# Performance work log

Measured on AMD Instinct MI355X. Metric: run time of the kernel, lower is better.

## Reference

```python
import jax, jax.numpy as jnp
import numpy as np

N_NODES = 50000
N_EDGES = 800000
HIDDEN = 128


def setup_inputs() -> dict:
    key = jax.random.key(0)
    k_emb, k_ei, k1, k2, k3, kb1, kb2, kb3 = jax.random.split(key, 8)
    emb = jax.random.normal(k_emb, (N_NODES, HIDDEN), dtype=jnp.float32)
    edge_index = jax.random.randint(k_ei, (2, N_EDGES), 0, N_NODES, dtype=jnp.int64)
    h = HIDDEN
    # MLP([2h, 4h, h, 1]) weights, Kaiming-uniform-ish init
    def lin(k, fan_in, fan_out):
        bound = 1.0 / np.sqrt(fan_in)
        return jax.random.uniform(k, (fan_in, fan_out), jnp.float32, -bound, bound)
    W1 = lin(k1, 2 * h, 4 * h)
    b1 = jax.random.uniform(kb1, (4 * h,), jnp.float32, -1.0 / np.sqrt(2 * h), 1.0 / np.sqrt(2 * h))
    W2 = lin(k2, 4 * h, h)
    b2 = jax.random.uniform(kb2, (h,), jnp.float32, -1.0 / np.sqrt(4 * h), 1.0 / np.sqrt(4 * h))
    W3 = lin(k3, h, 1)
    b3 = jax.random.uniform(kb3, (1,), jnp.float32, -1.0 / np.sqrt(h), 1.0 / np.sqrt(h))
    return {"emb": emb, "edge_index": edge_index,
            "W1": W1, "b1": b1, "W2": W2, "b2": b2, "W3": W3, "b3": b3}


def reference(emb, edge_index, W1, b1, W2, b2, W3, b3):
    # learn_edge_att=True path: gather endpoints, concat, 3-layer MLP
    col, row = edge_index[0], edge_index[1]
    f12 = jnp.concatenate([emb[col], emb[row]], axis=-1)  # [E, 2h]
    x = jax.nn.relu(f12 @ W1 + b1)                         # [E, 4h]
    x = jax.nn.relu(x @ W2 + b2)                           # [E, h]
    att_log_logits = x @ W3 + b3                           # [E, 1]
    return att_log_logits
```

## Files before the change

### kernel.cpp

```cpp
#include <hip/hip_runtime.h>
#include <hip/hip_bf16.h>
#include <stdint.h>

#define N_EDGES   800000
#define N_NODESC  50000
#define HID       128

typedef __attribute__((ext_vector_type(8))) short bf16x8;
typedef __attribute__((ext_vector_type(4))) float f32x4;
typedef __attribute__((ext_vector_type(4))) unsigned int u32x4;

__device__ __forceinline__ short f2bf(float f) {
    union { float f; uint32_t u; } v; v.f = f;
    uint32_t r = v.u + 0x7FFFu + ((v.u >> 16) & 1u);
    return (short)(r >> 16);
}

__device__ __forceinline__ uint32_t packbf2(float lo, float hi) {
    float2 t; t.x = lo; t.y = hi;
    __hip_bfloat162 h = __float22bfloat162_rn(t);
    uint32_t u;
    __builtin_memcpy(&u, &h, 4);
    return u;
}

__device__ __forceinline__ uint32_t addrelu2(uint32_t a, uint32_t b) {
    __hip_bfloat162 ha, hb;
    __builtin_memcpy(&ha, &a, 4);
    __builtin_memcpy(&hb, &b, 4);
    __hip_bfloat162 s = __hadd2(ha, hb);
    uint32_t x;
    __builtin_memcpy(&x, &s, 4);
    uint32_t neg = (x & 0x80008000u) >> 15;
    return x & ~(neg * 0xFFFFu);
}
__device__ __forceinline__ bf16x8 addrelu8(u32x4 p, u32x4 q) {
    u32x4 r;
    #pragma unroll
    for (int j = 0; j < 4; ++j) r[j] = addrelu2(p[j], q[j]);
    bf16x8 out;
    __builtin_memcpy(&out, &r, 16);
    return out;
}

#define PQ_OFF    0UL
#define W1S_OFF   102400000UL
#define W2S_OFF   (W1S_OFF + 262144UL)
#define CNT_OFF   (W2S_OFF + 131072UL)
#define BSUM_OFF  (CNT_OFF + 200704UL)
#define CUR_OFF   (BSUM_OFF + 1024UL)
#define SCOL_OFF  (CUR_OFF + 200704UL)
#define SROW_OFF  (SCOL_OFF + 3200000UL)
#define SID_OFF   (SROW_OFF + 3200000UL)

#define SCAN_BLOCKS 196

__global__ __launch_bounds__(256) void swizzle_kernel(const float* __restrict__ W1,
                                                      const float* __restrict__ W2,
                                                      short* __restrict__ W1s,
                                                      short* __restrict__ W2s) {
    int t = blockIdx.x * 256 + threadIdx.x;
    int lane = t & 63;
    int kq = lane >> 4;
    int nn = lane & 15;
    if (t < 16384) {
        int frag = t >> 6;
        int kc = frag >> 6;
        int nt = frag & 63;
        int n = nt * 16 + nn;
        int kbase = kc * 32 + kq * 8;
        bf16x8 v;
        #pragma unroll
        for (int j = 0; j < 8; ++j) {
            int k = kbase + j;
            float f = (n < 512) ? W1[k * 512 + n] : W1[(128 + k) * 512 + (n - 512)];
            v[j] = f2bf(f);
        }
        *(bf16x8*)(W1s + frag * 512 + lane * 8) = v;
    } else if (t < 24576) {
        int t2 = t - 16384;
        int frag = t2 >> 6;
        int kc = frag >> 3;
        int nt = frag & 7;
        int n = nt * 16 + nn;
        int kbase = kc * 32 + kq * 8;
        bf16x8 v;
        #pragma unroll
        for (int j = 0; j < 8; ++j) v[j] = f2bf(W2[(kbase + j) * HID + n]);
        *(bf16x8*)(W2s + frag * 512 + lane * 8) = v;
    }
}

__global__ __launch_bounds__(256) void precompute_kernel(const float* __restrict__ emb,
                                                         const short* __restrict__ W1s,
                                                         const float* __restrict__ b1,
                                                         short* __restrict__ PQ) {
    __shared__ short tile[4][16][272];
    int lane = threadIdx.x & 63;
    int w = threadIdx.x >> 6;
    int nb = blockIdx.x * 16;
    int m = lane & 15;
    int kq = lane >> 4;

    const float* arow = emb + (size_t)(nb + m) * 128 + kq * 8;

    f32x4 acc[16];
    #pragma unroll
    for (int i = 0; i < 16; ++i) acc[i] = (f32x4){0.f, 0.f, 0.f, 0.f};

    #pragma unroll
    for (int kc = 0; kc < 4; ++kc) {
        f32x4 x0 = *(const f32x4*)(arow + kc * 32);
        f32x4 x1 = *(const f32x4*)(arow + kc * 32 + 4);
        u32x4 au;
        au[0] = packbf2(x0[0], x0[1]); au[1] = packbf2(x0[2], x0[3]);
        au[2] = packbf2(x1[0], x1[1]); au[3] = packbf2(x1[2], x1[3]);
        bf16x8 a;
        __builtin_memcpy(&a, &au, 16);
        #pragma unroll
        for (int nt = 0; nt < 16; ++nt) {
            int frag = kc * 64 + (w * 16 + nt);
            bf16x8 b = *(const bf16x8*)(W1s + frag * 512 + lane * 8);
            acc[nt] = __builtin_amdgcn_mfma_f32_16x16x32_bf16(a, b, acc[nt], 0, 0, 0);
        }
    }

    #pragma unroll
    for (int nt = 0; nt < 16; ++nt) {
        int n = w * 256 + nt * 16 + m;
        float bias = (n < 512) ? b1[n] : 0.0f;
        #pragma unroll
        for (int r = 0; r < 4; ++r)
            tile[w][kq * 4 + r][nt * 16 + m] = f2bf(acc[nt][r] + bias);
    }

    #pragma unroll
    for (int s = 0; s < 8; ++s) {
        int row = s * 2 + (lane >> 5);
        int chunk = lane & 31;
        bf16x8 v = *(const bf16x8*)(&tile[w][row][chunk * 8]);
        *(bf16x8*)(PQ + (size_t)(nb + row) * 1024 + w * 256 + chunk * 8) = v;
    }
}


__global__ __launch_bounds__(256) void zero_kernel(int* __restrict__ counts) {
    counts[blockIdx.x * 256 + threadIdx.x] = 0;
}

__global__ __launch_bounds__(256) void hist_kernel(const int* __restrict__ ei,
                                                   int* __restrict__ counts) {
    int e = blockIdx.x * 256 + threadIdx.x;
    atomicAdd(&counts[ei[e]], 1);
}

__global__ __launch_bounds__(256) void scan1_kernel(const int* __restrict__ counts,
                                                    int* __restrict__ cursor,
                                                    int* __restrict__ blocksum) {
    __shared__ int sm[256];
    int t = threadIdx.x;
    int i = blockIdx.x * 256 + t;
    int v = counts[i];
    sm[t] = v;
    __syncthreads();
    #pragma unroll
    for (int off = 1; off < 256; off <<= 1) {
        int y = (t >= off) ? sm[t - off] : 0;
        __syncthreads();
        sm[t] += y;
        __syncthreads();
    }
    cursor[i] = sm[t] - v;
    if (t == 255) blocksum[blockIdx.x] = sm[t];
}

__global__ __launch_bounds__(256) void scan2_kernel(int* __restrict__ blocksum) {
    __shared__ int sm[256];
    int t = threadIdx.x;
    sm[t] = (t < SCAN_BLOCKS) ? blocksum[t] : 0;
    __syncthreads();
    if (t == 0) {
        int run = 0;
        for (int i = 0; i < SCAN_BLOCKS; ++i) { int c = sm[i]; sm[i] = run; run += c; }
    }
    __syncthreads();
    if (t < SCAN_BLOCKS) blocksum[t] = sm[t];
}

__global__ __launch_bounds__(256) void finalize_kernel(int* __restrict__ cursor,
                                                       const int* __restrict__ blockbase) {
    cursor[blockIdx.x * 256 + threadIdx.x] += blockbase[blockIdx.x];
}

__global__ __launch_bounds__(256) void scatter_kernel(const int* __restrict__ ei,
                                                      int* __restrict__ cursor,
                                                      int* __restrict__ scol,
                                                      int* __restrict__ srow,
                                                      int* __restrict__ sid) {
    int e = blockIdx.x * 256 + threadIdx.x;
    int c = ei[e];
    int r = ei[N_EDGES + e];
    int pos = atomicAdd(&cursor[c], 1);
    scol[pos] = c;
    srow[pos] = r;
    sid[pos]  = e;
}

__global__ __launch_bounds__(256, 2) void edge_kernel(const short* __restrict__ PQ,
                                                      const int* __restrict__ scol,
                                                      const int* __restrict__ srow,
                                                      const int* __restrict__ sid,
                                                      const short* __restrict__ W2s,
                                                      const float* __restrict__ b2,
                                                      const float* __restrict__ W3,
                                                      const float* __restrict__ b3,
                                                      float* __restrict__ out) {
    int lane = threadIdx.x & 63;
    int w = threadIdx.x >> 6;
    int e0 = blockIdx.x * 256 + w * 64;
    int m = lane & 15;
    int kq = lane >> 4;

    int idx_c = scol[e0 + lane];
    int idx_r = srow[e0 + lane];
    int idx_o = sid[e0 + lane];

    const short* pb[4];
    const short* qb[4];
    #pragma unroll
    for (int t = 0; t < 4; ++t) {
        int ce = __shfl(idx_c, t * 16 + m, 64);
        int re = __shfl(idx_r, t * 16 + m, 64);
        pb[t] = PQ + (size_t)ce * 1024 + kq * 8;
        qb[t] = PQ + (size_t)re * 1024 + 512 + kq * 8;
    }

    f32x4 acc[4][8];
    #pragma unroll
    for (int t = 0; t < 4; ++t)
        #pragma unroll
        for (int nt = 0; nt < 8; ++nt) acc[t][nt] = (f32x4){0.f, 0.f, 0.f, 0.f};

    #pragma unroll
    for (int kc = 0; kc < 16; ++kc) {
        u32x4 p[4], q[4];
        #pragma unroll
        for (int t = 0; t < 4; ++t) {
            p[t] = *(const u32x4*)(pb[t] + kc * 32);
            q[t] = *(const u32x4*)(qb[t] + kc * 32);
        }
        bf16x8 b[8];
        #pragma unroll
        for (int nt = 0; nt < 8; ++nt)
            b[nt] = *(const bf16x8*)(W2s + (kc * 8 + nt) * 512 + lane * 8);
        #pragma unroll
        for (int t = 0; t < 4; ++t) {
            bf16x8 a = addrelu8(p[t], q[t]);
            #pragma unroll
            for (int nt = 0; nt < 8; ++nt)
                acc[t][nt] = __builtin_amdgcn_mfma_f32_16x16x32_bf16(a, b[nt], acc[t][nt], 0, 0, 0);
        }
    }

    float b2v[8], w3v[8];
    #pragma unroll
    for (int nt = 0; nt < 8; ++nt) {
        b2v[nt] = b2[nt * 16 + m];
        w3v[nt] = W3[nt * 16 + m];
    }
    float b3s = b3[0];
    #pragma unroll
    for (int t = 0; t < 4; ++t) {
        float partial[4] = {0.f, 0.f, 0.f, 0.f};
        #pragma unroll
        for (int nt = 0; nt < 8; ++nt) {
            #pragma unroll
            for (int r = 0; r < 4; ++r) {
                float x2 = acc[t][nt][r] + b2v[nt];
                x2 = x2 > 0.f ? x2 : 0.f;
                partial[r] += x2 * w3v[nt];
            }
        }
        #pragma unroll
        for (int r = 0; r < 4; ++r) {
            #pragma unroll
            for (int off = 1; off < 16; off <<= 1)
                partial[r] += __shfl_xor(partial[r], off, 64);
            int oe = __shfl(idx_o, t * 16 + kq * 4 + r, 64);
            if (m == 0) out[oe] = partial[r] + b3s;
        }
    }
}

extern "C" void kernel_launch(void* const* d_in, const int* in_sizes, int n_in,
                              void* d_out, int out_size, void* d_ws, size_t ws_size,
                              hipStream_t stream) {
    const float* emb = (const float*)d_in[0];
    const int*   ei  = (const int*)d_in[1];
    const float* W1  = (const float*)d_in[2];
    const float* b1  = (const float*)d_in[3];
    const float* W2  = (const float*)d_in[4];
    const float* b2  = (const float*)d_in[5];
    const float* W3  = (const float*)d_in[6];
    const float* b3  = (const float*)d_in[7];
    float* out = (float*)d_out;

    short* PQ   = (short*)((char*)d_ws + PQ_OFF);
    short* W1s  = (short*)((char*)d_ws + W1S_OFF);
    short* W2s  = (short*)((char*)d_ws + W2S_OFF);
    int* counts = (int*)((char*)d_ws + CNT_OFF);
    int* bsum   = (int*)((char*)d_ws + BSUM_OFF);
    int* cursor = (int*)((char*)d_ws + CUR_OFF);
    int* scol   = (int*)((char*)d_ws + SCOL_OFF);
    int* srow   = (int*)((char*)d_ws + SROW_OFF);
    int* sid    = (int*)((char*)d_ws + SID_OFF);

    swizzle_kernel<<<96, 256, 0, stream>>>(W1, W2, W1s, W2s);
    zero_kernel<<<SCAN_BLOCKS, 256, 0, stream>>>(counts);
    hist_kernel<<<N_EDGES / 256, 256, 0, stream>>>(ei, counts);
    scan1_kernel<<<SCAN_BLOCKS, 256, 0, stream>>>(counts, cursor, bsum);
    scan2_kernel<<<1, 256, 0, stream>>>(bsum);
    finalize_kernel<<<SCAN_BLOCKS, 256, 0, stream>>>(cursor, bsum);
    scatter_kernel<<<N_EDGES / 256, 256, 0, stream>>>(ei, cursor, scol, srow, sid);

    precompute_kernel<<<N_NODESC / 16, 256, 0, stream>>>(emb, W1s, b1, PQ);
    edge_kernel<<<N_EDGES / 256, 256, 0, stream>>>(PQ, scol, srow, sid, W2s, b2, W3, b3, out);
}
```

Before: 449.4 us.

## Pack sorted edge indices into one word and permute outputs in a separate pass

The scatter step now writes one packed 32-bit word (row<<16 | col) per sorted edge plus a per-edge position array, replacing three separate index arrays. The edge kernel loads a single packed index, writes its results contiguously into a temporary buffer with vector stores, and a new permute kernel gathers them back into original edge order. The zero kernel is also replaced by hipMemsetAsync. This is meant to cut scattered writes and index traffic, at the cost of an extra launch and a gather pass. The packing relies on node ids fitting in 16 bits, which holds for 50000 nodes.

```diff
diff --git a/kernel.cpp b/kernel.cpp
--- a/kernel.cpp
+++ b/kernel.cpp
@@ -49,9 +49,9 @@
 #define CNT_OFF   (W2S_OFF + 131072UL)
 #define BSUM_OFF  (CNT_OFF + 200704UL)
 #define CUR_OFF   (BSUM_OFF + 1024UL)
-#define SCOL_OFF  (CUR_OFF + 200704UL)
-#define SROW_OFF  (SCOL_OFF + 3200000UL)
-#define SID_OFF   (SROW_OFF + 3200000UL)
+#define SPK_OFF   (CUR_OFF + 200704UL)
+#define POS_OFF   (SPK_OFF + 3200000UL)
+#define TMP_OFF   (POS_OFF + 3200000UL)
 
 #define SCAN_BLOCKS 196
 
@@ -144,10 +144,6 @@
 }
 
 
-__global__ __launch_bounds__(256) void zero_kernel(int* __restrict__ counts) {
-    counts[blockIdx.x * 256 + threadIdx.x] = 0;
-}
-
 __global__ __launch_bounds__(256) void hist_kernel(const int* __restrict__ ei,
                                                    int* __restrict__ counts) {
     int e = blockIdx.x * 256 + threadIdx.x;
@@ -194,43 +190,38 @@
 
 __global__ __launch_bounds__(256) void scatter_kernel(const int* __restrict__ ei,
                                                       int* __restrict__ cursor,
-                                                      int* __restrict__ scol,
-                                                      int* __restrict__ srow,
-                                                      int* __restrict__ sid) {
+                                                      unsigned int* __restrict__ spk,
+                                                      int* __restrict__ pos) {
     int e = blockIdx.x * 256 + threadIdx.x;
     int c = ei[e];
     int r = ei[N_EDGES + e];
-    int pos = atomicAdd(&cursor[c], 1);
-    scol[pos] = c;
-    srow[pos] = r;
-    sid[pos]  = e;
+    int p = atomicAdd(&cursor[c], 1);
+    spk[p] = ((unsigned int)r << 16) | (unsigned int)c;
+    pos[e] = p;
 }
 
 __global__ __launch_bounds__(256, 2) void edge_kernel(const short* __restrict__ PQ,
-                                                      const int* __restrict__ scol,
-                                                      const int* __restrict__ srow,
-                                                      const int* __restrict__ sid,
+                                                      const unsigned int* __restrict__ spk,
                                                       const short* __restrict__ W2s,
                                                       const float* __restrict__ b2,
                                                       const float* __restrict__ W3,
                                                       const float* __restrict__ b3,
-                                                      float* __restrict__ out) {
+                                                      float* __restrict__ tmp) {
     int lane = threadIdx.x & 63;
     int w = threadIdx.x >> 6;
     int e0 = blockIdx.x * 256 + w * 64;
     int m = lane & 15;
     int kq = lane >> 4;
 
-    int idx_c = scol[e0 + lane];
-    int idx_r = srow[e0 + lane];
-    int idx_o = sid[e0 + lane];
+    unsigned int pk = spk[e0 + lane];
 
     const short* pb[4];
     const short* qb[4];
     #pragma unroll
     for (int t = 0; t < 4; ++t) {
-        int ce = __shfl(idx_c, t * 16 + m, 64);
-        int re = __shfl(idx_r, t * 16 + m, 64);
+        unsigned int v = __shfl(pk, t * 16 + m, 64);
+        int ce = (int)(v & 0xFFFFu);
+        int re = (int)(v >> 16);
         pb[t] = PQ + (size_t)ce * 1024 + kq * 8;
         qb[t] = PQ + (size_t)re * 1024 + 512 + kq * 8;
     }
@@ -286,10 +277,21 @@
             #pragma unroll
             for (int off = 1; off < 16; off <<= 1)
                 partial[r] += __shfl_xor(partial[r], off, 64);
-            int oe = __shfl(idx_o, t * 16 + kq * 4 + r, 64);
-            if (m == 0) out[oe] = partial[r] + b3s;
-        }
-    }
+        }
+        if (m == 0) {
+            f32x4 v;
+            #pragma unroll
+            for (int r = 0; r < 4; ++r) v[r] = partial[r] + b3s;
+            *(f32x4*)(tmp + e0 + t * 16 + kq * 4) = v;
+        }
+    }
+}
+
+__global__ __launch_bounds__(256) void permute_kernel(const float* __restrict__ tmp,
+                                                      const int* __restrict__ pos,
+                                                      float* __restrict__ out) {
+    int e = blockIdx.x * 256 + threadIdx.x;
+    out[e] = tmp[pos[e]];
 }
 
 extern "C" void kernel_launch(void* const* d_in, const int* in_sizes, int n_in,
@@ -311,18 +313,19 @@
     int* counts = (int*)((char*)d_ws + CNT_OFF);
     int* bsum   = (int*)((char*)d_ws + BSUM_OFF);
     int* cursor = (int*)((char*)d_ws + CUR_OFF);
-    int* scol   = (int*)((char*)d_ws + SCOL_OFF);
-    int* srow   = (int*)((char*)d_ws + SROW_OFF);
-    int* sid    = (int*)((char*)d_ws + SID_OFF);
+    unsigned int* spk = (unsigned int*)((char*)d_ws + SPK_OFF);
+    int* pos    = (int*)((char*)d_ws + POS_OFF);
+    float* tmp  = (float*)((char*)d_ws + TMP_OFF);
 
     swizzle_kernel<<<96, 256, 0, stream>>>(W1, W2, W1s, W2s);
-    zero_kernel<<<SCAN_BLOCKS, 256, 0, stream>>>(counts);
+    hipMemsetAsync(counts, 0, SCAN_BLOCKS * 256 * sizeof(int), stream);
     hist_kernel<<<N_EDGES / 256, 256, 0, stream>>>(ei, counts);
     scan1_kernel<<<SCAN_BLOCKS, 256, 0, stream>>>(counts, cursor, bsum);
     scan2_kernel<<<1, 256, 0, stream>>>(bsum);
     finalize_kernel<<<SCAN_BLOCKS, 256, 0, stream>>>(cursor, bsum);
-    scatter_kernel<<<N_EDGES / 256, 256, 0, stream>>>(ei, cursor, scol, srow, sid);
+    scatter_kernel<<<N_EDGES / 256, 256, 0, stream>>>(ei, cursor, spk, pos);
 
     precompute_kernel<<<N_NODESC / 16, 256, 0, stream>>>(emb, W1s, b1, PQ);
-    edge_kernel<<<N_EDGES / 256, 256, 0, stream>>>(PQ, scol, srow, sid, W2s, b2, W3, b3, out);
-}
+    edge_kernel<<<N_EDGES / 256, 256, 0, stream>>>(PQ, spk, W2s, b2, W3, b3, tmp);
+    permute_kernel<<<N_EDGES / 256, 256, 0, stream>>>(tmp, pos, out);
+}
```

Result: no change. 457.7 us (+1.8%).
